# Kernel optimization log

Hardware: AMD Instinct MI355X
Metric: run time of the kernel (lower is better)

## Reference

```python
import jax, jax.numpy as jnp
import numpy as np
from jax import lax

EPS = 1e-8
ROOT_2 = 1.41421
STYLE_SIZE = 512
OUT_CH = 512
STYLE_SCALE = (2.0 / STYLE_SIZE) ** 0.5   # Weight_Scaling(style_size): equalized-LR sqrt(2/fan_in)
OUT_SCALE = (2.0 / (OUT_CH * 1 * 1)) ** 0.5  # Weight_Scaling(out_channels*1*1)


def setup_inputs() -> dict:
    key = jax.random.key(0)
    ks = jax.random.split(key, 10)
    B, Cin, Cout, H, S = 8, 512, 512, 32, 512
    return {
        "x": jax.random.normal(ks[0], (B, Cin, H, H), dtype=jnp.float32),
        "style_base": jax.random.normal(ks[1], (B, S), dtype=jnp.float32),
        "noise": jax.random.normal(ks[2], (B, 1, 2 * H, 2 * H), dtype=jnp.float32),
        "t": jax.random.normal(ks[3], (B, Cout, 2 * H, 2 * H), dtype=jnp.float32),
        # learned params
        "affine_w": jax.random.normal(ks[4], (Cin, S), dtype=jnp.float32) * (1.0 / np.sqrt(S)),
        "affine_b": jnp.zeros((Cin,), dtype=jnp.float32),
        "conv_w": jax.random.normal(ks[5], (Cout, Cin, 3, 3), dtype=jnp.float32),
        "conv_b": jnp.zeros((1, Cout, 1, 1), dtype=jnp.float32),
        "prelu_a": jnp.asarray(0.25, dtype=jnp.float32),
        "noise_scalar": jnp.zeros((1, Cout, 1, 1), dtype=jnp.float32) + 0.1,
        "out_w": jax.random.normal(ks[6], (3, Cout, 1, 1), dtype=jnp.float32) * (1.0 / np.sqrt(Cout)),
        "out_b": jnp.zeros((3,), dtype=jnp.float32),
    }


def reference(x, style_base, noise, t, affine_w, affine_b, conv_w, conv_b,
              prelu_a, noise_scalar, out_w, out_b):
    B, Cin, H, W = x.shape
    # style_std = affine(Weight_Scaling(style_base)) + 1  -> [B, Cin]
    style_std = (style_base * STYLE_SCALE) @ affine_w.T + affine_b + 1.0

    # bilinear x2 upsample (align_corners=False == half-pixel, matches jax.image.resize)
    x = jax.image.resize(x, (B, Cin, 2 * H, 2 * W), method="bilinear")

    # modulated conv with L2 demodulation, expressed as input-scale + conv + output-scale
    # per-sample weight w_b[o,i,k,l] = w[o,i,k,l]*s[b,i] / ||w*s||_b,o
    wsq = jnp.sum(conv_w ** 2, axis=(2, 3))                      # [O, I]
    demod = 1.0 / jnp.sqrt(jnp.einsum("oi,bi->bo", wsq, style_std ** 2) + EPS)  # [B, O]
    xm = x * style_std[:, :, None, None]
    y = lax.conv_general_dilated(xm, conv_w, (1, 1), "SAME",
                                 dimension_numbers=("NCHW", "OIHW", "NCHW"))
    y = y * demod[:, :, None, None] + conv_b + noise_scalar * noise
    # PReLU (single shared slope)
    y = jnp.where(y >= 0, y, prelu_a * y)

    # out branch: skip add, scale, toRGB 1x1 conv, clamp
    y = (y + t) / ROOT_2
    out = lax.conv_general_dilated(y * OUT_SCALE, out_w, (1, 1), "SAME",
                                   dimension_numbers=("NCHW", "OIHW", "NCHW"))
    out = jnp.clip(out + out_b[None, :, None, None], 0.0, 1.0)
    return (y, out)
```

## Files before the change

### kernel.cpp

```cpp
#include <hip/hip_runtime.h>


typedef short bf16x8 __attribute__((ext_vector_type(8)));
typedef short short8v __attribute__((ext_vector_type(8)));
typedef float f32x16 __attribute__((ext_vector_type(16)));

#define WS_STYLE 0
#define WS_DEMOD 16384
#define WS_WSQ   32768
#define WS_WPACK 1081344
#define WS_XM    5799936

__device__ __forceinline__ short f2bf(float f) {
  unsigned u = __float_as_uint(f);
  u += 0x7FFFu + ((u >> 16) & 1u);
  return (short)(u >> 16);
}

__device__ __forceinline__ void gld16(const short* g, char* l) {
  __builtin_amdgcn_global_load_lds((const __attribute__((address_space(1))) void*)g,
                                   (__attribute__((address_space(3))) void*)l,
                                   16, 0, 0);
}

__global__ void k_style(const float* __restrict__ sb, const float* __restrict__ aw,
                        const float* __restrict__ ab, float* __restrict__ style) {
  __shared__ float s_sb[512];
  int b = blockIdx.x;
  for (int i = threadIdx.x; i < 512; i += 256) s_sb[i] = sb[b * 512 + i] * 0.0625f;
  __syncthreads();
  for (int i = threadIdx.x; i < 512; i += 256) {
    const float4* wrow = (const float4*)(aw + (size_t)i * 512);
    float acc = 0.f;
    #pragma unroll 4
    for (int s4 = 0; s4 < 128; ++s4) {
      float4 w4 = wrow[s4];
      float4 sv = *(const float4*)(s_sb + s4 * 4);
      acc += w4.x * sv.x + w4.y * sv.y + w4.z * sv.z + w4.w * sv.w;
    }
    style[b * 512 + i] = acc + ab[i] + 1.0f;
  }
}

__global__ void k_wsq(const float* __restrict__ cw, float* __restrict__ wsq) {
  int idx = blockIdx.x * 256 + threadIdx.x;
  const float* p = cw + (size_t)idx * 9;
  float s = 0.f;
  #pragma unroll
  for (int j = 0; j < 9; ++j) s += p[j] * p[j];
  wsq[idx] = s;
}

__global__ void k_demod(const float* __restrict__ wsq, const float* __restrict__ style,
                        float* __restrict__ demod) {
  int wid = threadIdx.x >> 6, lane = threadIdx.x & 63;
  int idx = blockIdx.x * 4 + wid;
  int b = idx >> 9, o = idx & 511;
  const float* wr = wsq + (size_t)o * 512;
  const float* ss = style + b * 512;
  float sum = 0.f;
  #pragma unroll
  for (int k = 0; k < 8; ++k) {
    int i = k * 64 + lane;
    float s = ss[i];
    sum += wr[i] * s * s;
  }
  #pragma unroll
  for (int off = 32; off; off >>= 1) sum += __shfl_down(sum, off);
  if (lane == 0) demod[b * 512 + o] = rsqrtf(sum + 1e-8f);
}

__global__ void k_upsample(const float* __restrict__ x, const float* __restrict__ style,
                           short* __restrict__ xm) {
  int b = blockIdx.x / 66, hp = blockIdx.x % 66;
  short* xmp = xm + ((size_t)b * 66 + hp) * 66 * 512;
  if (hp == 0 || hp == 65) {
    short8v z = {0, 0, 0, 0, 0, 0, 0, 0};
    for (int u = threadIdx.x; u < 66 * 512 / 8; u += 256) ((short8v*)xmp)[u] = z;
    return;
  }
  int h = hp - 1;
  int j0 = (h >> 1) - 1 + (h & 1);
  float fj = (h & 1) ? 0.25f : 0.75f;
  int j0c = j0 < 0 ? 0 : j0;
  int j1c = j0 + 1 > 31 ? 31 : j0 + 1;
  __shared__ float xt[2][64][33];
  int ccc = threadIdx.x & 63;
  int wsub = threadIdx.x >> 6;
  for (int c0 = 0; c0 < 512; c0 += 64) {
    __syncthreads();
    #pragma unroll 4
    for (int k = 0; k < 16; ++k) {
      int idx = k * 256 + threadIdx.x;
      int ii = idx & 31, cc = (idx >> 5) & 63, jj = idx >> 11;
      xt[jj][cc][ii] = x[(((size_t)b * 512 + c0 + cc) * 32 + (jj ? j1c : j0c)) * 32 + ii];
    }
    __syncthreads();
    float sstyle = style[b * 512 + c0 + ccc];
    #pragma unroll 4
    for (int wk = 0; wk < 16; ++wk) {
      int w = wk * 4 + wsub;
      int i0 = (w >> 1) - 1 + (w & 1);
      float fi = (w & 1) ? 0.25f : 0.75f;
      int i0c = i0 < 0 ? 0 : i0;
      int i1c = i0 + 1 > 31 ? 31 : i0 + 1;
      float v0 = xt[0][ccc][i0c] * (1.f - fi) + xt[0][ccc][i1c] * fi;
      float v1 = xt[1][ccc][i0c] * (1.f - fi) + xt[1][ccc][i1c] * fi;
      float v = (v0 * (1.f - fj) + v1 * fj) * sstyle;
      xmp[(size_t)(w + 1) * 512 + c0 + ccc] = f2bf(v);
    }
    if (wsub == 0) {
      xmp[c0 + ccc] = 0;
      xmp[(size_t)65 * 512 + c0 + ccc] = 0;
    }
  }
}

__global__ void k_packw(const float* __restrict__ cw, short* __restrict__ wpk) {
  int unit = blockIdx.x * 256 + threadIdx.x;
  int s = unit >> 11;
  int rem = unit & 2047;
  int o = rem >> 2, sp = rem & 3;
  int tap = s >> 4, cc = s & 15;
  int i0 = cc * 32 + ((sp ^ ((o >> 1) & 3)) << 3);
  const float* src = cw + ((size_t)o * 512 + i0) * 9 + tap;
  short8v v;
  #pragma unroll
  for (int j = 0; j < 8; ++j) v[j] = f2bf(src[j * 9]);
  *(short8v*)(wpk + (size_t)unit * 8) = v;
}

__global__ __launch_bounds__(512, 2) void k_conv(
    const short* __restrict__ xm, const short* __restrict__ wpk,
    const float* __restrict__ demod, const float* __restrict__ convb,
    const float* __restrict__ nscal, const float* __restrict__ noise,
    const float* __restrict__ t, const float* __restrict__ prelu_a,
    float* __restrict__ y) {
  __shared__ char WTs[2][49152];
  __shared__ char XMs[2][25344];

  int tid = threadIdx.x;
  int bid = blockIdx.x;
  int cohalf = bid & 1, hq = (bid >> 1) & 15, b = bid >> 5;
  int wid = tid >> 6, lane = tid & 63;
  int wo = wid & 1, wsrow = wid >> 1;
  int l31 = lane & 31, lg = lane >> 5;

  const short* xb = xm + ((size_t)b * 66 + hq * 4) * 66 * 512;
  const short* wpkh = wpk + (size_t)cohalf * 256 * 32;
  int wb0 = ((wo * 128 + l31) << 6) + ((lg ^ ((l31 >> 1) & 3)) << 4);

  #pragma unroll
  for (int k = 0; k < 3; ++k) {
    int u = k * 512 + tid;
    int r = u / 264, rem = u - r * 264;
    int wp = rem >> 2, sp = rem & 3;
    gld16(xb + (size_t)(r * 66 + wp) * 512 + ((sp ^ ((wp >> 1) & 3)) << 3), XMs[0] + u * 16);
  }
  if (tid < 48) {
    int u = 1536 + tid;
    int rem = u - 1320;
    int wp = rem >> 2, sp = rem & 3;
    gld16(xb + (size_t)(5 * 66 + wp) * 512 + ((sp ^ ((wp >> 1) & 3)) << 3), XMs[0] + u * 16);
  }
  #pragma unroll
  for (int j = 0; j < 3; ++j) {
    const short* ws = wpkh + (size_t)(j * 16) * 16384;
    gld16(ws + tid * 8, WTs[0] + j * 16384 + tid * 16);
    gld16(ws + (512 + tid) * 8, WTs[0] + j * 16384 + (512 + tid) * 16);
  }

  f32x16 zf = {0,0,0,0,0,0,0,0,0,0,0,0,0,0,0,0};
  f32x16 acc[4][2];
  #pragma unroll
  for (int i = 0; i < 4; ++i) { acc[i][0] = zf; acc[i][1] = zf; }

  asm volatile("s_waitcnt vmcnt(0)" ::: "memory");
  __builtin_amdgcn_s_barrier();
  __builtin_amdgcn_sched_barrier(0);

  #pragma unroll 1
  for (int cc = 0; cc < 16; ++cc) {
    const char* XMc = XMs[cc & 1];
    char* XMn = (char*)XMs[(cc & 1) ^ 1];
    #pragma unroll
    for (int krow = 0; krow < 3; ++krow) {
      int g = cc * 3 + krow;
      const char* WTc = WTs[g & 1];
      char* WTn = (char*)WTs[(g & 1) ^ 1];

      if (g < 47) {
        int nkrow = (krow < 2) ? krow + 1 : 0;
        int ncc = (krow < 2) ? cc : cc + 1;
        #pragma unroll
        for (int j = 0; j < 3; ++j) {
          const short* ws = wpkh + (size_t)((nkrow * 3 + j) * 16 + ncc) * 16384;
          gld16(ws + tid * 8, WTn + j * 16384 + tid * 16);
          gld16(ws + (512 + tid) * 8, WTn + j * 16384 + (512 + tid) * 16);
        }
      }
      if (krow == 0 && cc < 15) {
        const short* xs = xb + (cc + 1) * 32;
        #pragma unroll
        for (int k = 0; k < 3; ++k) {
          int u = k * 512 + tid;
          int r = u / 264, rem = u - r * 264;
          int wp = rem >> 2, sp = rem & 3;
          gld16(xs + (size_t)(r * 66 + wp) * 512 + ((sp ^ ((wp >> 1) & 3)) << 3), XMn + u * 16);
        }
        if (tid < 48) {
          int u = 1536 + tid;
          int rem = u - 1320;
          int wp = rem >> 2, sp = rem & 3;
          gld16(xs + (size_t)(5 * 66 + wp) * 512 + ((sp ^ ((wp >> 1) & 3)) << 3), XMn + u * 16);
        }
      }

      #pragma unroll
      for (int j = 0; j < 3; ++j) {
        const char* Wp = WTc + j * 16384;
        bf16x8 wf0[4], wf1[4];
        #pragma unroll
        for (int cf = 0; cf < 4; ++cf) {
          wf0[cf] = *(const bf16x8*)(Wp + (wb0 + cf * 2048));
          wf1[cf] = *(const bf16x8*)(Wp + ((wb0 + cf * 2048) ^ 32));
        }
        int a = l31 + j;
        int xo = ((wsrow + krow) * 66 + a) * 64 + ((lg ^ ((a >> 1) & 3)) << 4);
        bf16x8 xf00 = *(const bf16x8*)(XMc + xo);
        bf16x8 xf01 = *(const bf16x8*)(XMc + xo + 2048);
        bf16x8 xf10 = *(const bf16x8*)(XMc + (xo ^ 32));
        bf16x8 xf11 = *(const bf16x8*)(XMc + ((xo ^ 32) + 2048));

        #pragma unroll
        for (int cf = 0; cf < 4; ++cf) {
          acc[cf][0] = __builtin_amdgcn_mfma_f32_32x32x16_bf16(wf0[cf], xf00, acc[cf][0], 0, 0, 0);
          acc[cf][1] = __builtin_amdgcn_mfma_f32_32x32x16_bf16(wf0[cf], xf01, acc[cf][1], 0, 0, 0);
        }
        #pragma unroll
        for (int cf = 0; cf < 4; ++cf) {
          acc[cf][0] = __builtin_amdgcn_mfma_f32_32x32x16_bf16(wf1[cf], xf10, acc[cf][0], 0, 0, 0);
          acc[cf][1] = __builtin_amdgcn_mfma_f32_32x32x16_bf16(wf1[cf], xf11, acc[cf][1], 0, 0, 0);
        }
      }

      asm volatile("s_waitcnt vmcnt(0)" ::: "memory");
      __builtin_amdgcn_s_barrier();
      __builtin_amdgcn_sched_barrier(0);
    }
  }

  float pa = prelu_a[0];
  const float inv_r2 = 1.0f / 1.41421f;
  int h = hq * 4 + wsrow;
  float nz0 = noise[((size_t)b * 64 + h) * 64 + l31];
  float nz1 = noise[((size_t)b * 64 + h) * 64 + 32 + l31];
  #pragma unroll
  for (int cf = 0; cf < 4; ++cf) {
    #pragma unroll
    for (int reg = 0; reg < 16; ++reg) {
      int orow = (reg & 3) + 8 * (reg >> 2) + 4 * lg;
      int o = cohalf * 256 + wo * 128 + cf * 32 + orow;
      float dm = demod[b * 512 + o];
      float cb = convb[o];
      float ns = nscal[o];
      #pragma unroll
      for (int sf = 0; sf < 2; ++sf) {
        int w = sf * 32 + l31;
        float v = acc[cf][sf][reg];
        v = v * dm + cb + ns * (sf ? nz1 : nz0);
        v = (v >= 0.f) ? v : pa * v;
        size_t oi = (((size_t)b * 512 + o) * 64 + h) * 64 + w;
        v = (v + t[oi]) * inv_r2;
        y[oi] = v;
      }
    }
  }
}

__global__ void k_rgb(const float* __restrict__ y, const float* __restrict__ ow,
                      const float* __restrict__ ob, float* __restrict__ out) {
  int b = blockIdx.x >> 6, h = blockIdx.x & 63;
  int w = threadIdx.x & 63, g = threadIdx.x >> 6;
  const float* yb = y + (((size_t)b * 512) * 64 + h) * 64 + w;
  float s0 = 0.f, s1 = 0.f, s2 = 0.f;
  for (int o = g * 128; o < g * 128 + 128; ++o) {
    float v = yb[(size_t)o * 4096];
    s0 += v * ow[o];
    s1 += v * ow[512 + o];
    s2 += v * ow[1024 + o];
  }
  __shared__ float red[3][4][64];
  red[0][g][w] = s0; red[1][g][w] = s1; red[2][g][w] = s2;
  __syncthreads();
  if (threadIdx.x < 192) {
    int c = threadIdx.x >> 6, ww = threadIdx.x & 63;
    float s = red[c][0][ww] + red[c][1][ww] + red[c][2][ww] + red[c][3][ww];
    s = s * 0.0625f + ob[c];
    s = fminf(fmaxf(s, 0.f), 1.f);
    out[(((size_t)b * 3 + c) * 64 + h) * 64 + ww] = s;
  }
}

extern "C" void kernel_launch(void* const* d_in, const int* in_sizes, int n_in,
                              void* d_out, int out_size, void* d_ws, size_t ws_size,
                              hipStream_t stream) {
  const float* x     = (const float*)d_in[0];
  const float* sb    = (const float*)d_in[1];
  const float* noise = (const float*)d_in[2];
  const float* t     = (const float*)d_in[3];
  const float* aw    = (const float*)d_in[4];
  const float* ab    = (const float*)d_in[5];
  const float* cw    = (const float*)d_in[6];
  const float* cb    = (const float*)d_in[7];
  const float* pa    = (const float*)d_in[8];
  const float* ns    = (const float*)d_in[9];
  const float* ow    = (const float*)d_in[10];
  const float* ob    = (const float*)d_in[11];
  char* ws = (char*)d_ws;
  float* style = (float*)(ws + WS_STYLE);
  float* demod = (float*)(ws + WS_DEMOD);
  float* wsq   = (float*)(ws + WS_WSQ);
  short* wpk   = (short*)(ws + WS_WPACK);
  short* xmw   = (short*)(ws + WS_XM);
  float* y   = (float*)d_out;
  float* out = y + 16777216;

  k_style<<<8, 256, 0, stream>>>(sb, aw, ab, style);
  k_wsq<<<1024, 256, 0, stream>>>(cw, wsq);
  k_demod<<<1024, 256, 0, stream>>>(wsq, style, demod);
  k_upsample<<<528, 256, 0, stream>>>(x, style, xmw);
  k_packw<<<1152, 256, 0, stream>>>(cw, wpk);
  k_conv<<<256, 512, 0, stream>>>(xmw, wpk, demod, cb, ns, noise, t, pa, y);
  k_rgb<<<512, 256, 0, stream>>>(y, ow, ob, out);
}
```

Baseline: 227.1 us.

## Software-pipeline LDS fragment reads across taps and across the barrier

```diff
diff --git a/kernel.cpp b/kernel.cpp
--- a/kernel.cpp
+++ b/kernel.cpp
@@ -130,6 +130,45 @@
   *(short8v*)(wpk + (size_t)unit * 8) = v;
 }
 
+#define DECL_SET(S) bf16x8 S##w00, S##w01, S##w02, S##w03, S##w10, S##w11, \
+                           S##w12, S##w13, S##x00, S##x01, S##x10, S##x11;
+
+#define READ_TAP(S, XMp, Wp, KROW, J) do {                                   \
+  S##w00 = *(const bf16x8*)((Wp) + wb0);                                     \
+  S##w01 = *(const bf16x8*)((Wp) + wb0 + 2048);                              \
+  S##w02 = *(const bf16x8*)((Wp) + wb0 + 4096);                              \
+  S##w03 = *(const bf16x8*)((Wp) + wb0 + 6144);                              \
+  S##w10 = *(const bf16x8*)((Wp) + (wb0 ^ 32));                              \
+  S##w11 = *(const bf16x8*)((Wp) + ((wb0 ^ 32) + 2048));                     \
+  S##w12 = *(const bf16x8*)((Wp) + ((wb0 ^ 32) + 4096));                     \
+  S##w13 = *(const bf16x8*)((Wp) + ((wb0 ^ 32) + 6144));                     \
+  { int a_ = l31 + (J);                                                      \
+    int xo_ = ((wsrow + (KROW)) * 66 + a_) * 64 + ((lg ^ ((a_ >> 1) & 3)) << 4); \
+    S##x00 = *(const bf16x8*)((XMp) + xo_);                                  \
+    S##x01 = *(const bf16x8*)((XMp) + xo_ + 2048);                           \
+    S##x10 = *(const bf16x8*)((XMp) + (xo_ ^ 32));                           \
+    S##x11 = *(const bf16x8*)((XMp) + ((xo_ ^ 32) + 2048)); }                \
+} while (0)
+
+#define MFMA_TAP(S) do {                                                     \
+  acc[0][0] = __builtin_amdgcn_mfma_f32_32x32x16_bf16(S##w00, S##x00, acc[0][0], 0, 0, 0); \
+  acc[0][1] = __builtin_amdgcn_mfma_f32_32x32x16_bf16(S##w00, S##x01, acc[0][1], 0, 0, 0); \
+  acc[1][0] = __builtin_amdgcn_mfma_f32_32x32x16_bf16(S##w01, S##x00, acc[1][0], 0, 0, 0); \
+  acc[1][1] = __builtin_amdgcn_mfma_f32_32x32x16_bf16(S##w01, S##x01, acc[1][1], 0, 0, 0); \
+  acc[2][0] = __builtin_amdgcn_mfma_f32_32x32x16_bf16(S##w02, S##x00, acc[2][0], 0, 0, 0); \
+  acc[2][1] = __builtin_amdgcn_mfma_f32_32x32x16_bf16(S##w02, S##x01, acc[2][1], 0, 0, 0); \
+  acc[3][0] = __builtin_amdgcn_mfma_f32_32x32x16_bf16(S##w03, S##x00, acc[3][0], 0, 0, 0); \
+  acc[3][1] = __builtin_amdgcn_mfma_f32_32x32x16_bf16(S##w03, S##x01, acc[3][1], 0, 0, 0); \
+  acc[0][0] = __builtin_amdgcn_mfma_f32_32x32x16_bf16(S##w10, S##x10, acc[0][0], 0, 0, 0); \
+  acc[0][1] = __builtin_amdgcn_mfma_f32_32x32x16_bf16(S##w10, S##x11, acc[0][1], 0, 0, 0); \
+  acc[1][0] = __builtin_amdgcn_mfma_f32_32x32x16_bf16(S##w11, S##x10, acc[1][0], 0, 0, 0); \
+  acc[1][1] = __builtin_amdgcn_mfma_f32_32x32x16_bf16(S##w11, S##x11, acc[1][1], 0, 0, 0); \
+  acc[2][0] = __builtin_amdgcn_mfma_f32_32x32x16_bf16(S##w12, S##x10, acc[2][0], 0, 0, 0); \
+  acc[2][1] = __builtin_amdgcn_mfma_f32_32x32x16_bf16(S##w12, S##x11, acc[2][1], 0, 0, 0); \
+  acc[3][0] = __builtin_amdgcn_mfma_f32_32x32x16_bf16(S##w13, S##x10, acc[3][0], 0, 0, 0); \
+  acc[3][1] = __builtin_amdgcn_mfma_f32_32x32x16_bf16(S##w13, S##x11, acc[3][1], 0, 0, 0); \
+} while (0)
+
 __global__ __launch_bounds__(512, 2) void k_conv(
     const short* __restrict__ xm, const short* __restrict__ wpk,
     const float* __restrict__ demod, const float* __restrict__ convb,
@@ -179,14 +218,17 @@
   __builtin_amdgcn_s_barrier();
   __builtin_amdgcn_sched_barrier(0);
 
+  DECL_SET(P) DECL_SET(A) DECL_SET(B)
+  READ_TAP(P, (const char*)XMs[0], (const char*)WTs[0], 0, 0);
+
   #pragma unroll 1
   for (int cc = 0; cc < 16; ++cc) {
-    const char* XMc = XMs[cc & 1];
+    const char* XMc = (const char*)XMs[cc & 1];
     char* XMn = (char*)XMs[(cc & 1) ^ 1];
     #pragma unroll
     for (int krow = 0; krow < 3; ++krow) {
       int g = cc * 3 + krow;
-      const char* WTc = WTs[g & 1];
+      const char* WTc = (const char*)WTs[g & 1];
       char* WTn = (char*)WTs[(g & 1) ^ 1];
 
       if (g < 47) {
@@ -216,37 +258,22 @@
         }
       }
 
-      #pragma unroll
-      for (int j = 0; j < 3; ++j) {
-        const char* Wp = WTc + j * 16384;
-        bf16x8 wf0[4], wf1[4];
-        #pragma unroll
-        for (int cf = 0; cf < 4; ++cf) {
-          wf0[cf] = *(const bf16x8*)(Wp + (wb0 + cf * 2048));
-          wf1[cf] = *(const bf16x8*)(Wp + ((wb0 + cf * 2048) ^ 32));
-        }
-        int a = l31 + j;
-        int xo = ((wsrow + krow) * 66 + a) * 64 + ((lg ^ ((a >> 1) & 3)) << 4);
-        bf16x8 xf00 = *(const bf16x8*)(XMc + xo);
-        bf16x8 xf01 = *(const bf16x8*)(XMc + xo + 2048);
-        bf16x8 xf10 = *(const bf16x8*)(XMc + (xo ^ 32));
-        bf16x8 xf11 = *(const bf16x8*)(XMc + ((xo ^ 32) + 2048));
-
-        #pragma unroll
-        for (int cf = 0; cf < 4; ++cf) {
-          acc[cf][0] = __builtin_amdgcn_mfma_f32_32x32x16_bf16(wf0[cf], xf00, acc[cf][0], 0, 0, 0);
-          acc[cf][1] = __builtin_amdgcn_mfma_f32_32x32x16_bf16(wf0[cf], xf01, acc[cf][1], 0, 0, 0);
-        }
-        #pragma unroll
-        for (int cf = 0; cf < 4; ++cf) {
-          acc[cf][0] = __builtin_amdgcn_mfma_f32_32x32x16_bf16(wf1[cf], xf10, acc[cf][0], 0, 0, 0);
-          acc[cf][1] = __builtin_amdgcn_mfma_f32_32x32x16_bf16(wf1[cf], xf11, acc[cf][1], 0, 0, 0);
-        }
+      READ_TAP(A, XMc, WTc + 16384, krow, 1);
+      MFMA_TAP(P);
+      READ_TAP(B, XMc, WTc + 32768, krow, 2);
+      MFMA_TAP(A);
+
+      asm volatile("s_waitcnt vmcnt(0) lgkmcnt(0)" ::: "memory");
+      __builtin_amdgcn_s_barrier();
+      if (g < 47) {
+        int nk = (krow < 2) ? krow + 1 : 0;
+        int ncc2 = (krow < 2) ? cc : cc + 1;
+        const char* XMc2 = (const char*)XMs[ncc2 & 1];
+        const char* WTc2 = (const char*)WTs[(g + 1) & 1];
+        READ_TAP(P, XMc2, WTc2, nk, 0);
       }
-
-      asm volatile("s_waitcnt vmcnt(0)" ::: "memory");
-      __builtin_amdgcn_s_barrier();
       __builtin_amdgcn_sched_barrier(0);
+      MFMA_TAP(B);
     }
   }
 
```

New measurement: 230.2 us. No clear change (+1.4%).

## Fuse toRGB 1x1 conv into conv epilogue with partial-sum reduction kernel

Applied to the files above, without the earlier changes.

```diff
diff --git a/kernel.cpp b/kernel.cpp
--- a/kernel.cpp
+++ b/kernel.cpp
@@ -10,6 +10,7 @@
 #define WS_WSQ   32768
 #define WS_WPACK 1081344
 #define WS_XM    5799936
+#define WS_PART  41484288
 
 __device__ __forceinline__ short f2bf(float f) {
   unsigned u = __float_as_uint(f);
@@ -135,6 +136,7 @@
     const float* __restrict__ demod, const float* __restrict__ convb,
     const float* __restrict__ nscal, const float* __restrict__ noise,
     const float* __restrict__ t, const float* __restrict__ prelu_a,
+    const float* __restrict__ ow, float* __restrict__ part,
     float* __restrict__ y) {
   __shared__ char WTs[2][49152];
   __shared__ char XMs[2][25344];
@@ -181,12 +183,12 @@
 
   #pragma unroll 1
   for (int cc = 0; cc < 16; ++cc) {
-    const char* XMc = XMs[cc & 1];
+    const char* XMc = (const char*)XMs[cc & 1];
     char* XMn = (char*)XMs[(cc & 1) ^ 1];
     #pragma unroll
     for (int krow = 0; krow < 3; ++krow) {
       int g = cc * 3 + krow;
-      const char* WTc = WTs[g & 1];
+      const char* WTc = (const char*)WTs[g & 1];
       char* WTn = (char*)WTs[(g & 1) ^ 1];
 
       if (g < 47) {
@@ -255,6 +257,7 @@
   int h = hq * 4 + wsrow;
   float nz0 = noise[((size_t)b * 64 + h) * 64 + l31];
   float nz1 = noise[((size_t)b * 64 + h) * 64 + 32 + l31];
+  float pr[3][2] = {{0.f, 0.f}, {0.f, 0.f}, {0.f, 0.f}};
   #pragma unroll
   for (int cf = 0; cf < 4; ++cf) {
     #pragma unroll
@@ -264,6 +267,7 @@
       float dm = demod[b * 512 + o];
       float cb = convb[o];
       float ns = nscal[o];
+      float w0 = ow[o], w1 = ow[512 + o], w2 = ow[1024 + o];
       #pragma unroll
       for (int sf = 0; sf < 2; ++sf) {
         int w = sf * 32 + l31;
@@ -273,33 +277,38 @@
         size_t oi = (((size_t)b * 512 + o) * 64 + h) * 64 + w;
         v = (v + t[oi]) * inv_r2;
         y[oi] = v;
+        pr[0][sf] += v * w0;
+        pr[1][sf] += v * w1;
+        pr[2][sf] += v * w2;
       }
     }
   }
-}
-
-__global__ void k_rgb(const float* __restrict__ y, const float* __restrict__ ow,
-                      const float* __restrict__ ob, float* __restrict__ out) {
-  int b = blockIdx.x >> 6, h = blockIdx.x & 63;
-  int w = threadIdx.x & 63, g = threadIdx.x >> 6;
-  const float* yb = y + (((size_t)b * 512) * 64 + h) * 64 + w;
-  float s0 = 0.f, s1 = 0.f, s2 = 0.f;
-  for (int o = g * 128; o < g * 128 + 128; ++o) {
-    float v = yb[(size_t)o * 4096];
-    s0 += v * ow[o];
-    s1 += v * ow[512 + o];
-    s2 += v * ow[1024 + o];
-  }
-  __shared__ float red[3][4][64];
-  red[0][g][w] = s0; red[1][g][w] = s1; red[2][g][w] = s2;
-  __syncthreads();
-  if (threadIdx.x < 192) {
-    int c = threadIdx.x >> 6, ww = threadIdx.x & 63;
-    float s = red[c][0][ww] + red[c][1][ww] + red[c][2][ww] + red[c][3][ww];
-    s = s * 0.0625f + ob[c];
-    s = fminf(fmaxf(s, 0.f), 1.f);
-    out[(((size_t)b * 3 + c) * 64 + h) * 64 + ww] = s;
-  }
+  #pragma unroll
+  for (int c = 0; c < 3; ++c) {
+    #pragma unroll
+    for (int sf = 0; sf < 2; ++sf)
+      pr[c][sf] += __shfl_down(pr[c][sf], 32);
+  }
+  if (lane < 32) {
+    int slice = cohalf * 2 + wo;
+    float* pp = part + (((size_t)(slice * 8 + b) * 3) * 64 + h) * 64;
+    #pragma unroll
+    for (int c = 0; c < 3; ++c) {
+      #pragma unroll
+      for (int sf = 0; sf < 2; ++sf)
+        pp[(size_t)c * 4096 + sf * 32 + l31] = pr[c][sf];
+    }
+  }
+}
+
+__global__ void k_rgbfin(const float* __restrict__ part, const float* __restrict__ ob,
+                         float* __restrict__ out) {
+  int idx = blockIdx.x * 256 + threadIdx.x;
+  int c = (idx / 4096) % 3;
+  float s = part[idx] + part[98304 + idx] + part[196608 + idx] + part[294912 + idx];
+  s = s * 0.0625f + ob[c];
+  s = fminf(fmaxf(s, 0.f), 1.f);
+  out[idx] = s;
 }
 
 extern "C" void kernel_launch(void* const* d_in, const int* in_sizes, int n_in,
@@ -323,6 +332,7 @@
   float* wsq   = (float*)(ws + WS_WSQ);
   short* wpk   = (short*)(ws + WS_WPACK);
   short* xmw   = (short*)(ws + WS_XM);
+  float* part  = (float*)(ws + WS_PART);
   float* y   = (float*)d_out;
   float* out = y + 16777216;
 
@@ -331,6 +341,6 @@
   k_demod<<<1024, 256, 0, stream>>>(wsq, style, demod);
   k_upsample<<<528, 256, 0, stream>>>(x, style, xmw);
   k_packw<<<1152, 256, 0, stream>>>(cw, wpk);
-  k_conv<<<256, 512, 0, stream>>>(xmw, wpk, demod, cb, ns, noise, t, pa, y);
-  k_rgb<<<512, 256, 0, stream>>>(y, ow, ob, out);
-}
+  k_conv<<<256, 512, 0, stream>>>(xmw, wpk, demod, cb, ns, noise, t, pa, ow, part, y);
+  k_rgbfin<<<384, 256, 0, stream>>>(part, ob, out);
+}
```

Result: faster. 220.8 us (-2.8%).
